# Optimization experiments

Hardware: AMD Instinct MI355X
Metric: run time of the kernel (lower is better)

The kernel has to match this reference:

```python
import jax, jax.numpy as jnp
import numpy as np

B, Cin, H, W = 8, 128, 64, 64
Cout, K, S, P = 128, 3, 1, 1
KK = K * K


def _conv(x, w, b=None):
    y = jax.lax.conv_general_dilated(
        x, w, window_strides=(S, S), padding=[(P, P), (P, P)],
        dimension_numbers=("NCHW", "OIHW", "NCHW"))
    if b is not None:
        y = y + b[None, :, None, None]
    return y


def setup_inputs() -> dict:
    key = jax.random.key(0)
    ks = jax.random.split(key, 6)
    x = jax.random.normal(ks[0], (B, Cin, H, W), jnp.float32)
    # offset/modulator convs are zero-init in the module; use small random
    # values so learned-offset sampling path is actually exercised.
    w_off = jax.random.normal(ks[1], (2 * KK, Cin, K, K), jnp.float32) * 0.01
    b_off = jax.random.normal(ks[2], (2 * KK,), jnp.float32) * 0.1
    w_mod = jax.random.normal(ks[3], (KK, Cin, K, K), jnp.float32) * 0.01
    b_mod = jax.random.normal(ks[4], (KK,), jnp.float32) * 0.1
    w_reg = jax.random.normal(ks[5], (Cout, Cin, K, K), jnp.float32) * (1.0 / np.sqrt(Cin * KK))
    return {"x": x, "w_off": w_off, "b_off": b_off,
            "w_mod": w_mod, "b_mod": b_mod, "w_reg": w_reg}


def _deform_conv2d(x, offset, mask, w_reg):
    # offset: [B, 2*KK, Hout, Wout] with (dy, dx) interleaved per tap (torchvision layout)
    Hout, Wout = offset.shape[2], offset.shape[3]
    off = offset.reshape(B, KK, 2, Hout, Wout)
    dy = off[:, :, 0].transpose(0, 2, 3, 1)  # [B,Hout,Wout,KK]
    dx = off[:, :, 1].transpose(0, 2, 3, 1)
    kh = (jnp.arange(KK) // K).astype(jnp.float32)
    kw = (jnp.arange(KK) % K).astype(jnp.float32)
    ho = jnp.arange(Hout, dtype=jnp.float32) * S - P
    wo = jnp.arange(Wout, dtype=jnp.float32) * S - P
    py = ho[None, :, None, None] + kh[None, None, None, :] + dy  # [B,Hout,Wout,KK]
    px = wo[None, None, :, None] + kw[None, None, None, :] + dx
    y0f = jnp.floor(py); x0f = jnp.floor(px)
    wy = (py - y0f)[..., None]; wx = (px - x0f)[..., None]
    y0 = y0f.astype(jnp.int32); x0 = x0f.astype(jnp.int32)
    x_bhwc = x.transpose(0, 2, 3, 1)  # [B,H,W,Cin]
    bidx = jnp.arange(B).reshape(B, 1, 1, 1)

    def gather(yi, xi):
        valid = ((yi >= 0) & (yi < H) & (xi >= 0) & (xi < W)).astype(x.dtype)
        v = x_bhwc[bidx, jnp.clip(yi, 0, H - 1), jnp.clip(xi, 0, W - 1)]
        return v * valid[..., None]  # [B,Hout,Wout,KK,Cin], zero outside

    v00 = gather(y0, x0)
    v01 = gather(y0, x0 + 1)
    v10 = gather(y0 + 1, x0)
    v11 = gather(y0 + 1, x0 + 1)
    val = (v00 * (1 - wy) * (1 - wx) + v01 * (1 - wy) * wx
           + v10 * wy * (1 - wx) + v11 * wy * wx)
    # modulated deformable conv v2: mask [B,KK,Hout,Wout]
    val = val * mask.transpose(0, 2, 3, 1)[..., None]
    # weighted accumulation over taps and input channels -> NCHW output
    return jnp.einsum("bhwkc,ock->bohw", val, w_reg.reshape(Cout, Cin, KK))


def reference(x, w_off, b_off, w_mod, b_mod, w_reg):
    offset = _conv(x, w_off, b_off)
    mask = 2.0 * jax.nn.sigmoid(_conv(x, w_mod, b_mod))
    return _deform_conv2d(x, offset, mask, w_reg)
```

## Files before the change

kernel.cpp:

```cpp
#include <hip/hip_runtime.h>
#include <hip/hip_bf16.h>
#include <math.h>

#define H 64
#define W 64
#define CIN 128
#define COUT 128
#define BATCH 8
#define NPIX (H*W)
#define PXT 32
#define AP  136
#define RP  36
#define VSZ (PXT*AP)

typedef __attribute__((ext_vector_type(8))) short bf16x8;
typedef __attribute__((ext_vector_type(4))) float f32x4;

static __device__ inline short f2bf(float f) {
  union { float f; unsigned u; } v; v.f = f;
  unsigned r = v.u + 0x7FFF + ((v.u >> 16) & 1);
  return (short)(r >> 16);
}
static __device__ inline float bf_lo(unsigned u) {
  union { unsigned u; float f; } v; v.u = u << 16; return v.f;
}
static __device__ inline float bf_hi(unsigned u) {
  union { unsigned u; float f; } v; v.u = u & 0xffff0000u; return v.f;
}

__global__ __launch_bounds__(256) void k_prep(const float* __restrict__ x,
    short* __restrict__ xbh,
    const float* __restrict__ w_off, const float* __restrict__ w_mod,
    short* __restrict__ wOMs, const float* __restrict__ w_reg,
    short* __restrict__ wAs) {
  __shared__ float tile[32][65];
  int blk = blockIdx.x;
  int t = threadIdx.x;
  if (blk < 2048) {
    int cg = blk & 3, y = (blk >> 2) & 63, b = blk >> 8;
#pragma unroll
    for (int j = 0; j < 8; ++j) {
      int idx = t + j * 256;
      int ci = idx >> 6, xi = idx & 63;
      tile[ci][xi] = x[(((b * CIN + cg * 32 + ci) * H + y) * W) + xi];
    }
    __syncthreads();
#pragma unroll
    for (int j = 0; j < 8; ++j) {
      int idx = t + j * 256;
      int xi = idx >> 5, ci = idx & 31;
      xbh[((b * H + y) * W + xi) * CIN + cg * 32 + ci] = f2bf(tile[ci][xi]);
    }
  } else if (blk < 2048 + 144) {
    int e = (blk - 2048) * 256 + t;
    int tap = e >> 12, oc = (e >> 7) & 31, c = e & 127;
    float v = 0.f;
    if (oc < 18)      v = w_off[(oc * 128 + c) * 9 + tap];
    else if (oc < 27) v = w_mod[((oc - 18) * 128 + c) * 9 + tap];
    int kb = c >> 5, quad = (c >> 3) & 3, j = c & 7;
    int g = oc >> 4, l16 = oc & 15;
    int o = ((tap * 4 + kb) * 2 + g) * 512 + (quad * 16 + l16) * 8 + j;
    wOMs[o] = f2bf(v);
  } else {
    int e = (blk - 2192) * 256 + t;
    int tap = e >> 14, oc = (e >> 7) & 127, c = e & 127;
    int kb = c >> 5, quad = (c >> 3) & 3, j = c & 7;
    int g = oc >> 4, l16 = oc & 15;
    int o = ((tap * 4 + kb) * 8 + g) * 512 + (quad * 16 + l16) * 8 + j;
    wAs[o] = f2bf(w_reg[(oc * 128 + c) * 9 + tap]);
  }
}

__global__ __launch_bounds__(512, 8) void k_deform(const short* __restrict__ xbh,
    const short* __restrict__ wOMs, const float* __restrict__ b_off,
    const float* __restrict__ b_mod, const short* __restrict__ wAs,
    float* __restrict__ out) {
  __shared__ __align__(16) char smem_u[31104];
  __shared__ __align__(16) float pw[PXT * 9 * 4];
  __shared__ __align__(16) int   pa[PXT * 9 * 4];
  float* red = (float*)smem_u;
  short* vs  = (short*)smem_u;

  int blk = blockIdx.x;
  int b = blk & 7, tile = blk >> 3;
  int pix0 = tile * PXT;
  int t = threadIdx.x;
  int lane = t & 63;
  int wv = t >> 6;
  int l16 = lane & 15, quad = lane >> 4;

  const short* xbB = xbh + (size_t)b * NPIX * CIN;

  {
    f32x4 acc_o[2][2] = {};
    for (int tap = wv; tap < 9; tap += 8) {
      const short* wt = wOMs + tap * 4096;
      int dy = tap / 3 - 1, dx = tap % 3 - 1;
      int lin[2], val[2];
#pragma unroll
      for (int nt = 0; nt < 2; ++nt) {
        int gp = pix0 + nt * 16 + l16;
        int y = (gp >> 6) + dy, x = (gp & 63) + dx;
        int ok = ((unsigned)y < H) && ((unsigned)x < W);
        val[nt] = ok;
        lin[nt] = ok ? ((y << 6) + x) : 0;
      }
#pragma unroll
      for (int kb = 0; kb < 4; ++kb) {
        bf16x8 a0 = *(const bf16x8*)&wt[(kb * 2 + 0) * 512 + lane * 8];
        bf16x8 a1 = *(const bf16x8*)&wt[(kb * 2 + 1) * 512 + lane * 8];
#pragma unroll
        for (int nt = 0; nt < 2; ++nt) {
          bf16x8 bv = *(const bf16x8*)&xbB[(size_t)lin[nt] * CIN + kb * 32 + quad * 8];
          if (!val[nt]) bv = (bf16x8){};
          acc_o[0][nt] = __builtin_amdgcn_mfma_f32_16x16x32_bf16(a0, bv, acc_o[0][nt], 0, 0, 0);
          acc_o[1][nt] = __builtin_amdgcn_mfma_f32_16x16x32_bf16(a1, bv, acc_o[1][nt], 0, 0, 0);
        }
      }
    }
#pragma unroll
    for (int mt = 0; mt < 2; ++mt)
#pragma unroll
      for (int nt = 0; nt < 2; ++nt)
#pragma unroll
        for (int r = 0; r < 4; ++r) {
          int oc = mt * 16 + quad * 4 + r;
          if (oc < 27) {
            int px = nt * 16 + l16;
            red[wv * (27 * RP) + oc * RP + px] = acc_o[mt][nt][r];
          }
        }
  }
  __syncthreads();

  for (int i = t; i < PXT * 9; i += 512) {
    int tap = i % 9, p = i / 9;
    float dyv = b_off[2 * tap], dxv = b_off[2 * tap + 1], z = b_mod[tap];
#pragma unroll
    for (int w = 0; w < 8; ++w) {
      const float* rw = red + w * (27 * RP);
      dyv += rw[(2 * tap) * RP + p];
      dxv += rw[(2 * tap + 1) * RP + p];
      z   += rw[(18 + tap) * RP + p];
    }
    float m = 2.f / (1.f + expf(-z));
    int gp = pix0 + p;
    float py = (float)((gp >> 6) - 1 + tap / 3) + dyv;
    float pxx = (float)((gp & 63) - 1 + tap % 3) + dxv;
    float yf = floorf(py), xf = floorf(pxx);
    float wy = py - yf, wx = pxx - xf;
    int y0 = (int)yf, x0 = (int)xf;
    int y1 = y0 + 1, x1 = x0 + 1;
    float vy0 = ((unsigned)y0 < H) ? 1.f : 0.f;
    float vy1 = ((unsigned)y1 < H) ? 1.f : 0.f;
    float vx0 = ((unsigned)x0 < W) ? 1.f : 0.f;
    float vx1 = ((unsigned)x1 < W) ? 1.f : 0.f;
    int y0c = min(max(y0, 0), H - 1), y1c = min(max(y1, 0), H - 1);
    int x0c = min(max(x0, 0), W - 1), x1c = min(max(x1, 0), W - 1);
    *(float4*)&pw[i * 4] = make_float4((1.f - wy) * (1.f - wx) * m * vy0 * vx0,
                                       (1.f - wy) * wx * m * vy0 * vx1,
                                       wy * (1.f - wx) * m * vy1 * vx0,
                                       wy * wx * m * vy1 * vx1);
    *(int4*)&pa[i * 4] = make_int4(((y0c << 6) + x0c) << 7,
                                   ((y0c << 6) + x1c) << 7,
                                   ((y1c << 6) + x0c) << 7,
                                   ((y1c << 6) + x1c) << 7);
  }
  __syncthreads();

  int ms = wv & 3, nh = wv >> 2;
  int cq = t & 15, ps = t >> 4;
  int c0 = cq * 8;

  f32x4 acc[2] = {};

  for (int tap = 0; tap < 9; ++tap) {
    short* vbuf = vs + (tap & 1) * VSZ;

    {
      int idx = (ps * 9 + tap) * 4;
      float4 wq = *(const float4*)&pw[idx];
      int4 aa = *(const int4*)&pa[idx];
      uint4 u00 = *(const uint4*)&xbB[aa.x + c0];
      uint4 u01 = *(const uint4*)&xbB[aa.y + c0];
      uint4 u10 = *(const uint4*)&xbB[aa.z + c0];
      uint4 u11 = *(const uint4*)&xbB[aa.w + c0];
      float s0 = wq.x * bf_lo(u00.x), s1 = wq.x * bf_hi(u00.x);
      float s2 = wq.x * bf_lo(u00.y), s3 = wq.x * bf_hi(u00.y);
      float s4 = wq.x * bf_lo(u00.z), s5 = wq.x * bf_hi(u00.z);
      float s6 = wq.x * bf_lo(u00.w), s7 = wq.x * bf_hi(u00.w);
      s0 = fmaf(wq.y, bf_lo(u01.x), s0); s1 = fmaf(wq.y, bf_hi(u01.x), s1);
      s2 = fmaf(wq.y, bf_lo(u01.y), s2); s3 = fmaf(wq.y, bf_hi(u01.y), s3);
      s4 = fmaf(wq.y, bf_lo(u01.z), s4); s5 = fmaf(wq.y, bf_hi(u01.z), s5);
      s6 = fmaf(wq.y, bf_lo(u01.w), s6); s7 = fmaf(wq.y, bf_hi(u01.w), s7);
      s0 = fmaf(wq.z, bf_lo(u10.x), s0); s1 = fmaf(wq.z, bf_hi(u10.x), s1);
      s2 = fmaf(wq.z, bf_lo(u10.y), s2); s3 = fmaf(wq.z, bf_hi(u10.y), s3);
      s4 = fmaf(wq.z, bf_lo(u10.z), s4); s5 = fmaf(wq.z, bf_hi(u10.z), s5);
      s6 = fmaf(wq.z, bf_lo(u10.w), s6); s7 = fmaf(wq.z, bf_hi(u10.w), s7);
      s0 = fmaf(wq.w, bf_lo(u11.x), s0); s1 = fmaf(wq.w, bf_hi(u11.x), s1);
      s2 = fmaf(wq.w, bf_lo(u11.y), s2); s3 = fmaf(wq.w, bf_hi(u11.y), s3);
      s4 = fmaf(wq.w, bf_lo(u11.z), s4); s5 = fmaf(wq.w, bf_hi(u11.z), s5);
      s6 = fmaf(wq.w, bf_lo(u11.w), s6); s7 = fmaf(wq.w, bf_hi(u11.w), s7);
      __hip_bfloat162 h0 = __float22bfloat162_rn(make_float2(s0, s1));
      __hip_bfloat162 h1 = __float22bfloat162_rn(make_float2(s2, s3));
      __hip_bfloat162 h2 = __float22bfloat162_rn(make_float2(s4, s5));
      __hip_bfloat162 h3 = __float22bfloat162_rn(make_float2(s6, s7));
      uint4 packed;
      packed.x = *(unsigned*)&h0; packed.y = *(unsigned*)&h1;
      packed.z = *(unsigned*)&h2; packed.w = *(unsigned*)&h3;
      *(uint4*)&vbuf[ps * AP + c0] = packed;
    }

    const short* wtap = wAs + tap * 16384;
    bf16x8 af0[4], af1[4];
#pragma unroll
    for (int kb = 0; kb < 4; ++kb) {
      af0[kb] = *(const bf16x8*)&wtap[(kb * 8 + ms * 2) * 512 + lane * 8];
      af1[kb] = *(const bf16x8*)&wtap[(kb * 8 + ms * 2 + 1) * 512 + lane * 8];
    }
    __syncthreads();

#pragma unroll
    for (int kb = 0; kb < 4; ++kb) {
      int kcol = kb * 32 + quad * 8;
      bf16x8 b0 = *(const bf16x8*)&vbuf[(nh * 16 + l16) * AP + kcol];
      acc[0] = __builtin_amdgcn_mfma_f32_16x16x32_bf16(af0[kb], b0, acc[0], 0, 0, 0);
      acc[1] = __builtin_amdgcn_mfma_f32_16x16x32_bf16(af1[kb], b0, acc[1], 0, 0, 0);
    }
  }

  int oc_base = ms * 32;
#pragma unroll
  for (int mt = 0; mt < 2; ++mt)
#pragma unroll
    for (int r = 0; r < 4; ++r) {
      int oc = oc_base + mt * 16 + quad * 4 + r;
      int px = nh * 16 + l16;
      out[(size_t)(b * COUT + oc) * NPIX + pix0 + px] = acc[mt][r];
    }
}

extern "C" void kernel_launch(void* const* d_in, const int* in_sizes, int n_in,
                              void* d_out, int out_size, void* d_ws, size_t ws_size,
                              hipStream_t stream) {
  const float* x     = (const float*)d_in[0];
  const float* w_off = (const float*)d_in[1];
  const float* b_off = (const float*)d_in[2];
  const float* w_mod = (const float*)d_in[3];
  const float* b_mod = (const float*)d_in[4];
  const float* w_reg = (const float*)d_in[5];

  short* xbh  = (short*)d_ws;
  short* wAs  = xbh + 4194304;
  short* wOMs = wAs + 147456;
  float* out  = (float*)d_out;

  k_prep<<<dim3(2768), 256, 0, stream>>>(x, xbh, w_off, w_mod, wOMs,
                                         w_reg, wAs);
  k_deform<<<dim3(NPIX / PXT * BATCH), 512, 0, stream>>>(
      xbh, wOMs, b_off, b_mod, wAs, out);
}
```

Before: 117.4 us.

## Double pixel tile to 64 so each wave reuses weight fragments across two N-tiles

Raises the pixel tile per block from 32 to 64. Each wave now computes two 16-pixel MFMA column tiles, so every weight A-fragment loaded from global memory feeds twice as many MFMAs. Each thread gathers and interpolates 16 channels instead of 8. The offset/mask conv is split into two pixel halves with four waves each, and the reduction is adjusted to match. The trade-off is half as many blocks, more LDS per block and a lower occupancy bound (launch bounds 512,4), which can leave fewer blocks to hide gather latency.

```diff
diff --git a/kernel.cpp b/kernel.cpp
--- a/kernel.cpp
+++ b/kernel.cpp
@@ -8,7 +8,7 @@
 #define COUT 128
 #define BATCH 8
 #define NPIX (H*W)
-#define PXT 32
+#define PXT 64
 #define AP  136
 #define RP  36
 #define VSZ (PXT*AP)
@@ -71,11 +71,11 @@
   }
 }
 
-__global__ __launch_bounds__(512, 8) void k_deform(const short* __restrict__ xbh,
+__global__ __launch_bounds__(512, 4) void k_deform(const short* __restrict__ xbh,
     const short* __restrict__ wOMs, const float* __restrict__ b_off,
     const float* __restrict__ b_mod, const short* __restrict__ wAs,
     float* __restrict__ out) {
-  __shared__ __align__(16) char smem_u[31104];
+  __shared__ __align__(16) char smem_u[2 * VSZ * 2];
   __shared__ __align__(16) float pw[PXT * 9 * 4];
   __shared__ __align__(16) int   pa[PXT * 9 * 4];
   float* red = (float*)smem_u;
@@ -92,14 +92,19 @@
   const short* xbB = xbh + (size_t)b * NPIX * CIN;
 
   {
+    int h = wv >> 2, tg = wv & 3;
+    int pix0h = pix0 + h * 32;
     f32x4 acc_o[2][2] = {};
-    for (int tap = wv; tap < 9; tap += 8) {
+#pragma unroll
+    for (int ti = 0; ti < 3; ++ti) {
+      int tap = tg + ti * 4;
+      if (tap > 8) break;
       const short* wt = wOMs + tap * 4096;
       int dy = tap / 3 - 1, dx = tap % 3 - 1;
       int lin[2], val[2];
 #pragma unroll
       for (int nt = 0; nt < 2; ++nt) {
-        int gp = pix0 + nt * 16 + l16;
+        int gp = pix0h + nt * 16 + l16;
         int y = (gp >> 6) + dy, x = (gp & 63) + dx;
         int ok = ((unsigned)y < H) && ((unsigned)x < W);
         val[nt] = ok;
@@ -135,13 +140,14 @@
 
   for (int i = t; i < PXT * 9; i += 512) {
     int tap = i % 9, p = i / 9;
+    int h = p >> 5, pl = p & 31;
     float dyv = b_off[2 * tap], dxv = b_off[2 * tap + 1], z = b_mod[tap];
 #pragma unroll
-    for (int w = 0; w < 8; ++w) {
-      const float* rw = red + w * (27 * RP);
-      dyv += rw[(2 * tap) * RP + p];
-      dxv += rw[(2 * tap + 1) * RP + p];
-      z   += rw[(18 + tap) * RP + p];
+    for (int w = 0; w < 4; ++w) {
+      const float* rw = red + (4 * h + w) * (27 * RP);
+      dyv += rw[(2 * tap) * RP + pl];
+      dxv += rw[(2 * tap + 1) * RP + pl];
+      z   += rw[(18 + tap) * RP + pl];
     }
     float m = 2.f / (1.f + expf(-z));
     int gp = pix0 + p;
@@ -169,10 +175,10 @@
   __syncthreads();
 
   int ms = wv & 3, nh = wv >> 2;
-  int cq = t & 15, ps = t >> 4;
-  int c0 = cq * 8;
-
-  f32x4 acc[2] = {};
+  int cq = t & 7, ps = t >> 3;
+  int c0 = cq * 16;
+
+  f32x4 acc[2][2] = {};
 
   for (int tap = 0; tap < 9; ++tap) {
     short* vbuf = vs + (tap & 1) * VSZ;
@@ -181,34 +187,50 @@
       int idx = (ps * 9 + tap) * 4;
       float4 wq = *(const float4*)&pw[idx];
       int4 aa = *(const int4*)&pa[idx];
-      uint4 u00 = *(const uint4*)&xbB[aa.x + c0];
-      uint4 u01 = *(const uint4*)&xbB[aa.y + c0];
-      uint4 u10 = *(const uint4*)&xbB[aa.z + c0];
-      uint4 u11 = *(const uint4*)&xbB[aa.w + c0];
-      float s0 = wq.x * bf_lo(u00.x), s1 = wq.x * bf_hi(u00.x);
-      float s2 = wq.x * bf_lo(u00.y), s3 = wq.x * bf_hi(u00.y);
-      float s4 = wq.x * bf_lo(u00.z), s5 = wq.x * bf_hi(u00.z);
-      float s6 = wq.x * bf_lo(u00.w), s7 = wq.x * bf_hi(u00.w);
-      s0 = fmaf(wq.y, bf_lo(u01.x), s0); s1 = fmaf(wq.y, bf_hi(u01.x), s1);
-      s2 = fmaf(wq.y, bf_lo(u01.y), s2); s3 = fmaf(wq.y, bf_hi(u01.y), s3);
-      s4 = fmaf(wq.y, bf_lo(u01.z), s4); s5 = fmaf(wq.y, bf_hi(u01.z), s5);
-      s6 = fmaf(wq.y, bf_lo(u01.w), s6); s7 = fmaf(wq.y, bf_hi(u01.w), s7);
-      s0 = fmaf(wq.z, bf_lo(u10.x), s0); s1 = fmaf(wq.z, bf_hi(u10.x), s1);
-      s2 = fmaf(wq.z, bf_lo(u10.y), s2); s3 = fmaf(wq.z, bf_hi(u10.y), s3);
-      s4 = fmaf(wq.z, bf_lo(u10.z), s4); s5 = fmaf(wq.z, bf_hi(u10.z), s5);
-      s6 = fmaf(wq.z, bf_lo(u10.w), s6); s7 = fmaf(wq.z, bf_hi(u10.w), s7);
-      s0 = fmaf(wq.w, bf_lo(u11.x), s0); s1 = fmaf(wq.w, bf_hi(u11.x), s1);
-      s2 = fmaf(wq.w, bf_lo(u11.y), s2); s3 = fmaf(wq.w, bf_hi(u11.y), s3);
-      s4 = fmaf(wq.w, bf_lo(u11.z), s4); s5 = fmaf(wq.w, bf_hi(u11.z), s5);
-      s6 = fmaf(wq.w, bf_lo(u11.w), s6); s7 = fmaf(wq.w, bf_hi(u11.w), s7);
-      __hip_bfloat162 h0 = __float22bfloat162_rn(make_float2(s0, s1));
-      __hip_bfloat162 h1 = __float22bfloat162_rn(make_float2(s2, s3));
-      __hip_bfloat162 h2 = __float22bfloat162_rn(make_float2(s4, s5));
-      __hip_bfloat162 h3 = __float22bfloat162_rn(make_float2(s6, s7));
-      uint4 packed;
-      packed.x = *(unsigned*)&h0; packed.y = *(unsigned*)&h1;
-      packed.z = *(unsigned*)&h2; packed.w = *(unsigned*)&h3;
-      *(uint4*)&vbuf[ps * AP + c0] = packed;
+      uint4 a_lo = *(const uint4*)&xbB[aa.x + c0];
+      uint4 a_hi = *(const uint4*)&xbB[aa.x + c0 + 8];
+      uint4 b_lo = *(const uint4*)&xbB[aa.y + c0];
+      uint4 b_hi = *(const uint4*)&xbB[aa.y + c0 + 8];
+      uint4 c_lo = *(const uint4*)&xbB[aa.z + c0];
+      uint4 c_hi = *(const uint4*)&xbB[aa.z + c0 + 8];
+      uint4 d_lo = *(const uint4*)&xbB[aa.w + c0];
+      uint4 d_hi = *(const uint4*)&xbB[aa.w + c0 + 8];
+      float s[16];
+#pragma unroll
+      for (int j = 0; j < 4; ++j) {
+        unsigned ua = ((const unsigned*)&a_lo)[j];
+        unsigned ub = ((const unsigned*)&b_lo)[j];
+        unsigned uc = ((const unsigned*)&c_lo)[j];
+        unsigned ud = ((const unsigned*)&d_lo)[j];
+        s[2*j]   = fmaf(wq.w, bf_lo(ud), fmaf(wq.z, bf_lo(uc),
+                   fmaf(wq.y, bf_lo(ub), wq.x * bf_lo(ua))));
+        s[2*j+1] = fmaf(wq.w, bf_hi(ud), fmaf(wq.z, bf_hi(uc),
+                   fmaf(wq.y, bf_hi(ub), wq.x * bf_hi(ua))));
+      }
+#pragma unroll
+      for (int j = 0; j < 4; ++j) {
+        unsigned ua = ((const unsigned*)&a_hi)[j];
+        unsigned ub = ((const unsigned*)&b_hi)[j];
+        unsigned uc = ((const unsigned*)&c_hi)[j];
+        unsigned ud = ((const unsigned*)&d_hi)[j];
+        s[8+2*j]   = fmaf(wq.w, bf_lo(ud), fmaf(wq.z, bf_lo(uc),
+                     fmaf(wq.y, bf_lo(ub), wq.x * bf_lo(ua))));
+        s[8+2*j+1] = fmaf(wq.w, bf_hi(ud), fmaf(wq.z, bf_hi(uc),
+                     fmaf(wq.y, bf_hi(ub), wq.x * bf_hi(ua))));
+      }
+      uint4 p0, p1;
+#pragma unroll
+      for (int j = 0; j < 4; ++j) {
+        __hip_bfloat162 h2 = __float22bfloat162_rn(make_float2(s[2*j], s[2*j+1]));
+        ((unsigned*)&p0)[j] = *(unsigned*)&h2;
+      }
+#pragma unroll
+      for (int j = 0; j < 4; ++j) {
+        __hip_bfloat162 h2 = __float22bfloat162_rn(make_float2(s[8+2*j], s[8+2*j+1]));
+        ((unsigned*)&p1)[j] = *(unsigned*)&h2;
+      }
+      *(uint4*)&vbuf[ps * AP + c0] = p0;
+      *(uint4*)&vbuf[ps * AP + c0 + 8] = p1;
     }
 
     const short* wtap = wAs + tap * 16384;
@@ -223,9 +245,12 @@
 #pragma unroll
     for (int kb = 0; kb < 4; ++kb) {
       int kcol = kb * 32 + quad * 8;
-      bf16x8 b0 = *(const bf16x8*)&vbuf[(nh * 16 + l16) * AP + kcol];
-      acc[0] = __builtin_amdgcn_mfma_f32_16x16x32_bf16(af0[kb], b0, acc[0], 0, 0, 0);
-      acc[1] = __builtin_amdgcn_mfma_f32_16x16x32_bf16(af1[kb], b0, acc[1], 0, 0, 0);
+      bf16x8 b0 = *(const bf16x8*)&vbuf[(nh * 32 + l16) * AP + kcol];
+      bf16x8 b1 = *(const bf16x8*)&vbuf[(nh * 32 + 16 + l16) * AP + kcol];
+      acc[0][0] = __builtin_amdgcn_mfma_f32_16x16x32_bf16(af0[kb], b0, acc[0][0], 0, 0, 0);
+      acc[0][1] = __builtin_amdgcn_mfma_f32_16x16x32_bf16(af0[kb], b1, acc[0][1], 0, 0, 0);
+      acc[1][0] = __builtin_amdgcn_mfma_f32_16x16x32_bf16(af1[kb], b0, acc[1][0], 0, 0, 0);
+      acc[1][1] = __builtin_amdgcn_mfma_f32_16x16x32_bf16(af1[kb], b1, acc[1][1], 0, 0, 0);
     }
   }
 
@@ -233,11 +258,13 @@
 #pragma unroll
   for (int mt = 0; mt < 2; ++mt)
 #pragma unroll
-    for (int r = 0; r < 4; ++r) {
-      int oc = oc_base + mt * 16 + quad * 4 + r;
-      int px = nh * 16 + l16;
-      out[(size_t)(b * COUT + oc) * NPIX + pix0 + px] = acc[mt][r];
-    }
+    for (int nt = 0; nt < 2; ++nt)
+#pragma unroll
+      for (int r = 0; r < 4; ++r) {
+        int oc = oc_base + mt * 16 + quad * 4 + r;
+        int px = nh * 32 + nt * 16 + l16;
+        out[(size_t)(b * COUT + oc) * NPIX + pix0 + px] = acc[mt][nt][r];
+      }
 }
 
 extern "C" void kernel_launch(void* const* d_in, const int* in_sizes, int n_in,
```

Result: no change. 116.5 us (-0.8%).

## Switch deform conv MFMA to 32x32x16 tiles with split-K reduction

Applied to the files above, without the earlier changes.

Replaces the 16x16x32 bf16 MFMA tiles with 32x32x16 tiles in both the offset/mask conv and the main deformable GEMM, repacking the weight layouts in the prep kernel to match. The main GEMM now splits K across two wave groups and sums the partial results through shared memory before the store. Gather addresses are stored as 16-bit pixel indices to shrink shared memory, and the bilinear interpolation loop is compacted. The aim is fewer MFMA and fragment-load instructions per tile. The cost is an extra reduction pass with barriers and half the waves staying idle during the final store.

```diff
diff --git a/kernel.cpp b/kernel.cpp
--- a/kernel.cpp
+++ b/kernel.cpp
@@ -15,6 +15,7 @@
 
 typedef __attribute__((ext_vector_type(8))) short bf16x8;
 typedef __attribute__((ext_vector_type(4))) float f32x4;
+typedef __attribute__((ext_vector_type(16))) float f32x16;
 
 static __device__ inline short f2bf(float f) {
   union { float f; unsigned u; } v; v.f = f;
@@ -57,16 +58,17 @@
     float v = 0.f;
     if (oc < 18)      v = w_off[(oc * 128 + c) * 9 + tap];
     else if (oc < 27) v = w_mod[((oc - 18) * 128 + c) * 9 + tap];
-    int kb = c >> 5, quad = (c >> 3) & 3, j = c & 7;
-    int g = oc >> 4, l16 = oc & 15;
-    int o = ((tap * 4 + kb) * 2 + g) * 512 + (quad * 16 + l16) * 8 + j;
+    int kstep = c >> 4, g = (c >> 3) & 1, j = c & 7;
+    int lane = g * 32 + oc;
+    int o = ((tap * 8 + kstep) * 64 + lane) * 8 + j;
     wOMs[o] = f2bf(v);
   } else {
     int e = (blk - 2192) * 256 + t;
     int tap = e >> 14, oc = (e >> 7) & 127, c = e & 127;
-    int kb = c >> 5, quad = (c >> 3) & 3, j = c & 7;
-    int g = oc >> 4, l16 = oc & 15;
-    int o = ((tap * 4 + kb) * 8 + g) * 512 + (quad * 16 + l16) * 8 + j;
+    int kstep = c >> 4, g = (c >> 3) & 1, j = c & 7;
+    int ms = oc >> 5, m = oc & 31;
+    int lane = g * 32 + m;
+    int o = (((tap * 8 + kstep) * 4 + ms) * 64 + lane) * 8 + j;
     wAs[o] = f2bf(w_reg[(oc * 128 + c) * 9 + tap]);
   }
 }
@@ -76,10 +78,11 @@
     const float* __restrict__ b_mod, const short* __restrict__ wAs,
     float* __restrict__ out) {
   __shared__ __align__(16) char smem_u[31104];
-  __shared__ __align__(16) float pw[PXT * 9 * 4];
-  __shared__ __align__(16) int   pa[PXT * 9 * 4];
-  float* red = (float*)smem_u;
-  short* vs  = (short*)smem_u;
+  __shared__ __align__(16) float  pw[PXT * 9 * 4];
+  __shared__ __align__(16) ushort pa4[PXT * 9 * 4];
+  float* red  = (float*)smem_u;
+  short* vs   = (short*)smem_u;
+  float* redE = (float*)smem_u;
 
   int blk = blockIdx.x;
   int b = blk & 7, tile = blk >> 3;
@@ -87,49 +90,36 @@
   int t = threadIdx.x;
   int lane = t & 63;
   int wv = t >> 6;
-  int l16 = lane & 15, quad = lane >> 4;
+  int n32 = lane & 31, g = lane >> 5;
 
   const short* xbB = xbh + (size_t)b * NPIX * CIN;
 
   {
-    f32x4 acc_o[2][2] = {};
-    for (int tap = wv; tap < 9; tap += 8) {
-      const short* wt = wOMs + tap * 4096;
+    f32x16 accO = {};
+#pragma unroll
+    for (int ti = 0; ti < 2; ++ti) {
+      int tap = wv + ti * 8;
+      if (tap > 8) break;
       int dy = tap / 3 - 1, dx = tap % 3 - 1;
-      int lin[2], val[2];
-#pragma unroll
-      for (int nt = 0; nt < 2; ++nt) {
-        int gp = pix0 + nt * 16 + l16;
-        int y = (gp >> 6) + dy, x = (gp & 63) + dx;
-        int ok = ((unsigned)y < H) && ((unsigned)x < W);
-        val[nt] = ok;
-        lin[nt] = ok ? ((y << 6) + x) : 0;
+      int gp = pix0 + n32;
+      int y = (gp >> 6) + dy, x = (gp & 63) + dx;
+      int ok = ((unsigned)y < H) && ((unsigned)x < W);
+      int lin = ok ? ((y << 6) + x) : 0;
+      const short* wt = wOMs;
+#pragma unroll
+      for (int kstep = 0; kstep < 8; ++kstep) {
+        bf16x8 a = *(const bf16x8*)&wt[((tap * 8 + kstep) * 64 + lane) * 8];
+        int c0 = kstep * 16 + g * 8;
+        bf16x8 bv = *(const bf16x8*)&xbB[(size_t)lin * CIN + c0];
+        if (!ok) bv = (bf16x8){};
+        accO = __builtin_amdgcn_mfma_f32_32x32x16_bf16(a, bv, accO, 0, 0, 0);
       }
-#pragma unroll
-      for (int kb = 0; kb < 4; ++kb) {
-        bf16x8 a0 = *(const bf16x8*)&wt[(kb * 2 + 0) * 512 + lane * 8];
-        bf16x8 a1 = *(const bf16x8*)&wt[(kb * 2 + 1) * 512 + lane * 8];
-#pragma unroll
-        for (int nt = 0; nt < 2; ++nt) {
-          bf16x8 bv = *(const bf16x8*)&xbB[(size_t)lin[nt] * CIN + kb * 32 + quad * 8];
-          if (!val[nt]) bv = (bf16x8){};
-          acc_o[0][nt] = __builtin_amdgcn_mfma_f32_16x16x32_bf16(a0, bv, acc_o[0][nt], 0, 0, 0);
-          acc_o[1][nt] = __builtin_amdgcn_mfma_f32_16x16x32_bf16(a1, bv, acc_o[1][nt], 0, 0, 0);
-        }
-      }
-    }
-#pragma unroll
-    for (int mt = 0; mt < 2; ++mt)
-#pragma unroll
-      for (int nt = 0; nt < 2; ++nt)
-#pragma unroll
-        for (int r = 0; r < 4; ++r) {
-          int oc = mt * 16 + quad * 4 + r;
-          if (oc < 27) {
-            int px = nt * 16 + l16;
-            red[wv * (27 * RP) + oc * RP + px] = acc_o[mt][nt][r];
-          }
-        }
+    }
+#pragma unroll
+    for (int r = 0; r < 16; ++r) {
+      int row = (r & 3) + 8 * (r >> 2) + 4 * g;
+      if (row < 27) red[wv * (27 * RP) + row * RP + n32] = accO[r];
+    }
   }
   __syncthreads();
 
@@ -161,18 +151,18 @@
                                        (1.f - wy) * wx * m * vy0 * vx1,
                                        wy * (1.f - wx) * m * vy1 * vx0,
                                        wy * wx * m * vy1 * vx1);
-    *(int4*)&pa[i * 4] = make_int4(((y0c << 6) + x0c) << 7,
-                                   ((y0c << 6) + x1c) << 7,
-                                   ((y1c << 6) + x0c) << 7,
-                                   ((y1c << 6) + x1c) << 7);
-  }
-  __syncthreads();
-
-  int ms = wv & 3, nh = wv >> 2;
+    pa4[i * 4 + 0] = (ushort)((y0c << 6) + x0c);
+    pa4[i * 4 + 1] = (ushort)((y0c << 6) + x1c);
+    pa4[i * 4 + 2] = (ushort)((y1c << 6) + x0c);
+    pa4[i * 4 + 3] = (ushort)((y1c << 6) + x1c);
+  }
+  __syncthreads();
+
+  int ms = wv & 3, ks = wv >> 2;
   int cq = t & 15, ps = t >> 4;
-  int c0 = cq * 8;
-
-  f32x4 acc[2] = {};
+  int c0s = cq * 8;
+
+  f32x16 acc = {};
 
   for (int tap = 0; tap < 9; ++tap) {
     short* vbuf = vs + (tap & 1) * VSZ;
@@ -180,64 +170,65 @@
     {
       int idx = (ps * 9 + tap) * 4;
       float4 wq = *(const float4*)&pw[idx];
-      int4 aa = *(const int4*)&pa[idx];
-      uint4 u00 = *(const uint4*)&xbB[aa.x + c0];
-      uint4 u01 = *(const uint4*)&xbB[aa.y + c0];
-      uint4 u10 = *(const uint4*)&xbB[aa.z + c0];
-      uint4 u11 = *(const uint4*)&xbB[aa.w + c0];
-      float s0 = wq.x * bf_lo(u00.x), s1 = wq.x * bf_hi(u00.x);
-      float s2 = wq.x * bf_lo(u00.y), s3 = wq.x * bf_hi(u00.y);
-      float s4 = wq.x * bf_lo(u00.z), s5 = wq.x * bf_hi(u00.z);
-      float s6 = wq.x * bf_lo(u00.w), s7 = wq.x * bf_hi(u00.w);
-      s0 = fmaf(wq.y, bf_lo(u01.x), s0); s1 = fmaf(wq.y, bf_hi(u01.x), s1);
-      s2 = fmaf(wq.y, bf_lo(u01.y), s2); s3 = fmaf(wq.y, bf_hi(u01.y), s3);
-      s4 = fmaf(wq.y, bf_lo(u01.z), s4); s5 = fmaf(wq.y, bf_hi(u01.z), s5);
-      s6 = fmaf(wq.y, bf_lo(u01.w), s6); s7 = fmaf(wq.y, bf_hi(u01.w), s7);
-      s0 = fmaf(wq.z, bf_lo(u10.x), s0); s1 = fmaf(wq.z, bf_hi(u10.x), s1);
-      s2 = fmaf(wq.z, bf_lo(u10.y), s2); s3 = fmaf(wq.z, bf_hi(u10.y), s3);
-      s4 = fmaf(wq.z, bf_lo(u10.z), s4); s5 = fmaf(wq.z, bf_hi(u10.z), s5);
-      s6 = fmaf(wq.z, bf_lo(u10.w), s6); s7 = fmaf(wq.z, bf_hi(u10.w), s7);
-      s0 = fmaf(wq.w, bf_lo(u11.x), s0); s1 = fmaf(wq.w, bf_hi(u11.x), s1);
-      s2 = fmaf(wq.w, bf_lo(u11.y), s2); s3 = fmaf(wq.w, bf_hi(u11.y), s3);
-      s4 = fmaf(wq.w, bf_lo(u11.z), s4); s5 = fmaf(wq.w, bf_hi(u11.z), s5);
-      s6 = fmaf(wq.w, bf_lo(u11.w), s6); s7 = fmaf(wq.w, bf_hi(u11.w), s7);
-      __hip_bfloat162 h0 = __float22bfloat162_rn(make_float2(s0, s1));
-      __hip_bfloat162 h1 = __float22bfloat162_rn(make_float2(s2, s3));
-      __hip_bfloat162 h2 = __float22bfloat162_rn(make_float2(s4, s5));
-      __hip_bfloat162 h3 = __float22bfloat162_rn(make_float2(s6, s7));
+      int a00 = (int)pa4[idx]     * CIN;
+      int a01 = (int)pa4[idx + 1] * CIN;
+      int a10 = (int)pa4[idx + 2] * CIN;
+      int a11 = (int)pa4[idx + 3] * CIN;
+      uint4 u00 = *(const uint4*)&xbB[a00 + c0s];
+      uint4 u01 = *(const uint4*)&xbB[a01 + c0s];
+      uint4 u10 = *(const uint4*)&xbB[a10 + c0s];
+      uint4 u11 = *(const uint4*)&xbB[a11 + c0s];
       uint4 packed;
-      packed.x = *(unsigned*)&h0; packed.y = *(unsigned*)&h1;
-      packed.z = *(unsigned*)&h2; packed.w = *(unsigned*)&h3;
-      *(uint4*)&vbuf[ps * AP + c0] = packed;
-    }
-
-    const short* wtap = wAs + tap * 16384;
-    bf16x8 af0[4], af1[4];
-#pragma unroll
-    for (int kb = 0; kb < 4; ++kb) {
-      af0[kb] = *(const bf16x8*)&wtap[(kb * 8 + ms * 2) * 512 + lane * 8];
-      af1[kb] = *(const bf16x8*)&wtap[(kb * 8 + ms * 2 + 1) * 512 + lane * 8];
+#pragma unroll
+      for (int j = 0; j < 4; ++j) {
+        unsigned ua = ((const unsigned*)&u00)[j];
+        unsigned ub = ((const unsigned*)&u01)[j];
+        unsigned uc = ((const unsigned*)&u10)[j];
+        unsigned ud = ((const unsigned*)&u11)[j];
+        float s0 = fmaf(wq.w, bf_lo(ud), fmaf(wq.z, bf_lo(uc),
+                   fmaf(wq.y, bf_lo(ub), wq.x * bf_lo(ua))));
+        float s1 = fmaf(wq.w, bf_hi(ud), fmaf(wq.z, bf_hi(uc),
+                   fmaf(wq.y, bf_hi(ub), wq.x * bf_hi(ua))));
+        __hip_bfloat162 h2 = __float22bfloat162_rn(make_float2(s0, s1));
+        ((unsigned*)&packed)[j] = *(unsigned*)&h2;
+      }
+      *(uint4*)&vbuf[ps * AP + c0s] = packed;
+    }
+
+    bf16x8 af[4];
+#pragma unroll
+    for (int i = 0; i < 4; ++i) {
+      int kstep = ks * 4 + i;
+      af[i] = *(const bf16x8*)&wAs[(((tap * 8 + kstep) * 4 + ms) * 64 + lane) * 8];
     }
     __syncthreads();
 
 #pragma unroll
-    for (int kb = 0; kb < 4; ++kb) {
-      int kcol = kb * 32 + quad * 8;
-      bf16x8 b0 = *(const bf16x8*)&vbuf[(nh * 16 + l16) * AP + kcol];
-      acc[0] = __builtin_amdgcn_mfma_f32_16x16x32_bf16(af0[kb], b0, acc[0], 0, 0, 0);
-      acc[1] = __builtin_amdgcn_mfma_f32_16x16x32_bf16(af1[kb], b0, acc[1], 0, 0, 0);
-    }
-  }
-
-  int oc_base = ms * 32;
-#pragma unroll
-  for (int mt = 0; mt < 2; ++mt)
-#pragma unroll
-    for (int r = 0; r < 4; ++r) {
-      int oc = oc_base + mt * 16 + quad * 4 + r;
-      int px = nh * 16 + l16;
-      out[(size_t)(b * COUT + oc) * NPIX + pix0 + px] = acc[mt][r];
-    }
+    for (int i = 0; i < 4; ++i) {
+      int kstep = ks * 4 + i;
+      int c0 = kstep * 16 + g * 8;
+      bf16x8 bfr = *(const bf16x8*)&vbuf[n32 * AP + c0];
+      acc = __builtin_amdgcn_mfma_f32_32x32x16_bf16(af[i], bfr, acc, 0, 0, 0);
+    }
+  }
+
+  __syncthreads();
+  if (ks == 1) {
+#pragma unroll
+    for (int r = 0; r < 16; ++r) {
+      int row = (r & 3) + 8 * (r >> 2) + 4 * g;
+      redE[ms * (32 * 33) + row * 33 + n32] = acc[r];
+    }
+  }
+  __syncthreads();
+  if (ks == 0) {
+#pragma unroll
+    for (int r = 0; r < 16; ++r) {
+      int row = (r & 3) + 8 * (r >> 2) + 4 * g;
+      float v = acc[r] + redE[ms * (32 * 33) + row * 33 + n32];
+      out[(size_t)(b * COUT + ms * 32 + row) * NPIX + pix0 + n32] = v;
+    }
+  }
 }
 
 extern "C" void kernel_launch(void* const* d_in, const int* in_sizes, int n_in,
```

Measured after the change: 112.1 us. -4.6%, faster.
